# Performance work log

Hardware: AMD Instinct MI355X
Metric: run time of the kernel (lower is better)

The kernel has to match this reference:

```python
import jax, jax.numpy as jnp
import numpy as np

K = 16          # max_points
S = 3           # num_scales
DM = 256        # d_model
KD = 16         # k_dim geometric projection
TAU = 1e-4
LN_EPS = 1e-5


def _boundaries():
    edges = [(i, j) for i in range(K) for j in range(i + 1, K)]
    tris = [(i, j, k) for i in range(K) for j in range(i + 1, K) for k in range(j + 1, K)]
    E, T = len(edges), len(tris)
    B1 = np.zeros((K, E), np.float32)
    for e, (i, j) in enumerate(edges):
        B1[i, e] = -1.0
        B1[j, e] = 1.0
    eidx = {e: n for n, e in enumerate(edges)}
    B2 = np.zeros((E, T), np.float32)
    for t, (i, j, k) in enumerate(tris):
        B2[eidx[(j, k)], t] = 1.0
        B2[eidx[(i, k)], t] = -1.0
        B2[eidx[(i, j)], t] = 1.0
    ei = np.array([e[0] for e in edges])
    ej = np.array([e[1] for e in edges])
    tij = np.array([eidx[(a, b)] for a, b, c in tris])
    tjk = np.array([eidx[(b, c)] for a, b, c in tris])
    tik = np.array([eidx[(a, c)] for a, b, c in tris])
    return (jnp.asarray(B1), jnp.asarray(B2), jnp.asarray(np.abs(B1)),
            jnp.asarray(ei), jnp.asarray(ej), jnp.asarray(tij), jnp.asarray(tjk), jnp.asarray(tik))

_B1, _B2, _ABS, _EI, _EJ, _TIJ, _TJK, _TIK = _boundaries()
E = _B1.shape[1]  # 120


def _ln(x, g, b):
    m = jnp.mean(x, -1, keepdims=True)
    v = jnp.mean((x - m) ** 2, -1, keepdims=True)
    return (x - m) * jax.lax.rsqrt(v + LN_EPS) * g + b


def setup_inputs() -> dict:
    key = jax.random.key(0)
    ks = jax.random.split(key, 12)
    B = 1024
    p = lambda k, *sh: 0.02 * jax.random.normal(k, sh, dtype=jnp.float32)
    return {
        'x': jax.random.normal(ks[0], (B, K, DM), dtype=jnp.float32),
        'mask': jnp.ones((B, K), dtype=jnp.float32),
        'Wg': p(ks[1], DM, KD), 'bg': jnp.zeros((KD,), jnp.float32),
        'log_scales': jnp.linspace(-1.5, 1.5, S, dtype=jnp.float32),
        'Wv': p(ks[2], DM, DM * S), 'bv': jnp.zeros((DM * S,), jnp.float32),
        'We': p(ks[3], DM, DM * S), 'be': jnp.zeros((DM * S,), jnp.float32),
        'Wo': p(ks[4], DM * S * 2, DM), 'bo': jnp.zeros((DM,), jnp.float32),
        'ln1_g': jnp.ones((DM,), jnp.float32), 'ln1_b': jnp.zeros((DM,), jnp.float32),
        'ln2_g': jnp.ones((DM,), jnp.float32), 'ln2_b': jnp.zeros((DM,), jnp.float32),
        'Wf1': p(ks[5], DM, DM * 4), 'bf1': jnp.zeros((DM * 4,), jnp.float32),
        'Wf2': p(ks[6], DM * 4, DM), 'bf2': jnp.zeros((DM,), jnp.float32),
    }


def reference(x, mask, Wg, bg, log_scales, Wv, bv, We, be, Wo, bo,
              ln1_g, ln1_b, ln2_g, ln2_b, Wf1, bf1, Wf2, bf2):
    B = x.shape[0]
    xn = _ln(x, ln1_g, ln1_b)
    P = xn @ Wg + bg                                   # [B,K,KD]
    m2 = mask[:, :, None] * mask[:, None, :]           # [B,K,K]
    p2 = jnp.sum(P * P, -1)
    Dsq = jnp.maximum(p2[:, :, None] + p2[:, None, :] - 2.0 * jnp.einsum('bkc,blc->bkl', P, P), 0.0) * m2
    sig2 = jnp.exp(log_scales) ** 2                    # [S]
    V0 = (xn @ Wv + bv).reshape(B, K, S, DM).transpose(0, 2, 1, 3)   # [B,S,K,D]
    Eraw = jnp.einsum('ke,bkd->bed', _ABS, xn)         # [B,E,D]
    Ein = (Eraw @ We + be).reshape(B, E, S, DM).transpose(0, 2, 1, 3)  # [B,S,E,D]
    aff = jnp.exp(-Dsq[:, None] / (2.0 * sig2[None, :, None, None] + 1e-8)) * m2[:, None]  # [B,S,K,K]
    W1 = aff[:, :, _EI, _EJ]                           # [B,S,E]
    W2 = W1[:, :, _TIJ] * W1[:, :, _TJK] * W1[:, :, _TIK]  # [B,S,T]
    L0 = jnp.einsum('ke,bse,le->bskl', _B1, W1, _B1) + TAU * jnp.eye(K, dtype=x.dtype)
    node_upd = jnp.einsum('bskl,bsld->bskd', L0, V0)
    term_down = jnp.einsum('ke,bk,kf->bef', _B1, mask, _B1)
    term_up = jnp.einsum('et,bst,ft->bsef', _B2, W2, _B2)
    L1 = term_down[:, None] + term_up + TAU * jnp.eye(E, dtype=x.dtype)
    edge_msg = jnp.einsum('bsef,bsfd->bsed', L1, Ein)
    edge_upd = jnp.einsum('ke,bsed->bskd', _ABS, edge_msg)
    nu = node_upd.transpose(0, 2, 1, 3).reshape(B, K, S * DM)
    eu = edge_upd.transpose(0, 2, 1, 3).reshape(B, K, S * DM)
    x = x + (jnp.concatenate([nu, eu], -1) @ Wo + bo)  # residual + attn_out (dropout=eval noop)
    h = _ln(x, ln2_g, ln2_b)
    return x + (jax.nn.gelu(h @ Wf1 + bf1, approximate=False) @ Wf2 + bf2)
```

## Files before the change

kernel.cpp:

```cpp
#include <hip/hip_runtime.h>
#include <hip/hip_bf16.h>
#include <cstdint>
#include <cstddef>

#define TAU 1e-4f
#define LN_EPS 1e-5f

typedef unsigned short ushort_t;
typedef unsigned int uint_t;
typedef __attribute__((ext_vector_type(8))) short short8;
typedef __attribute__((ext_vector_type(4))) float f32x4;

__device__ __forceinline__ ushort_t f2bf(float f) {
    union { float f; unsigned int u; } c; c.f = f;
    unsigned int r = (c.u + 0x7fffu + ((c.u >> 16) & 1u)) >> 16;
    return (ushort_t)r;
}
__device__ __forceinline__ float bf2f(ushort_t u) {
    union { unsigned int u; float f; } c; c.u = ((unsigned int)u) << 16;
    return c.f;
}
__device__ __forceinline__ void glds16(const void* g, void* l) {
    __builtin_amdgcn_global_load_lds((const __attribute__((address_space(1))) unsigned int*)g,
                                     (__attribute__((address_space(3))) unsigned int*)l,
                                     16, 0, 0);
}

__global__ __launch_bounds__(256) void kprep(
    const float* __restrict__ Wv, const float* __restrict__ We,
    const float* __restrict__ Wo, const float* __restrict__ bv,
    const float* __restrict__ be, const float* __restrict__ Wf1,
    const float* __restrict__ Wf2, ushort_t* __restrict__ WkT,
    ushort_t* __restrict__ Wf1T, ushort_t* __restrict__ Wf2T,
    float* __restrict__ cvpart, float* __restrict__ beWo) {
    __shared__ __align__(16) float S[64 * 65];
    const int tid = threadIdx.x;
    const int id = blockIdx.x;
    if (id < 384) {
        float (*rowS)[256] = (float(*)[256])S;
        const int q0 = (id & 63) * 4;
        const int w = id >> 6;
        const int half = w / 3, s = w - half * 3;
        const float* src = half ? We : Wv;
#pragma unroll
        for (int r = 0; r < 4; ++r)
            rowS[r][tid] = src[(size_t)(q0 + r) * 768 + s * 256 + tid];
        __syncthreads();
        const float* wo = Wo + (size_t)(half * 768 + s * 256) * 256 + tid;
        float a0 = 0.f, a1 = 0.f, a2 = 0.f, a3 = 0.f;
        for (int d = 0; d < 256; ++d) {
            float wv = wo[(size_t)d * 256];
            a0 += rowS[0][d] * wv; a1 += rowS[1][d] * wv;
            a2 += rowS[2][d] * wv; a3 += rowS[3][d] * wv;
        }
        const int rt = half * 3 + s;
        ushort4 pk;
        pk.x = f2bf(a0); pk.y = f2bf(a1); pk.z = f2bf(a2); pk.w = f2bf(a3);
        *(ushort4*)&WkT[(size_t)(rt * 256 + tid) * 256 + q0] = pk;
    } else if (id < 390) {
        const int w = id - 384;
        const int half = w / 3, s = w - half * 3;
        const float* vec = half ? be : bv;
        S[tid] = vec[s * 256 + tid];
        __syncthreads();
        const float* wo = Wo + (size_t)(half * 768 + s * 256) * 256 + tid;
        float acc = 0.f;
        for (int d = 0; d < 256; ++d) acc += S[d] * wo[(size_t)d * 256];
        if (half) beWo[s * 256 + tid] = acc;
        else cvpart[s * 256 + tid] = acc;
    } else {
        float (*tS)[65] = (float(*)[65])S;
        const float* src; ushort_t* dst;
        int sr0, sc0, ss, dr0, dc0, ds_;
        if (id < 454) {
            int t = id - 390; int ki = t & 3, ni = t >> 2;
            src = Wf1; ss = 1024; sr0 = ki * 64; sc0 = ni * 64;
            dst = Wf1T; ds_ = 256; dr0 = ni * 64; dc0 = ki * 64;
        } else {
            int t = id - 454; int ki = t >> 2, ni = t & 3;
            src = Wf2; ss = 256; sr0 = ki * 64; sc0 = ni * 64;
            dst = Wf2T; ds_ = 1024; dr0 = ni * 64; dc0 = ki * 64;
        }
        const int rl = tid >> 6, cl = tid & 63;
#pragma unroll
        for (int p = 0; p < 16; ++p) {
            int r = p * 4 + rl;
            tS[r][cl] = src[(size_t)(sr0 + r) * ss + sc0 + cl];
        }
        __syncthreads();
#pragma unroll
        for (int p = 0; p < 16; ++p) {
            int r = p * 4 + rl;
            dst[(size_t)(dr0 + r) * ds_ + dc0 + cl] = f2bf(tS[cl][r]);
        }
    }
}

__global__ __launch_bounds__(256) void kLN1G(
    const float* __restrict__ xg, const float* __restrict__ maskg,
    const float* __restrict__ Wg, const float* __restrict__ bg,
    const float* __restrict__ ls, const float* __restrict__ g1,
    const float* __restrict__ b1, ushort_t* __restrict__ xnbuf,
    float* __restrict__ Mbuf, float* __restrict__ gbuf) {
    __shared__ float XS[16][260];
    __shared__ __align__(16) float WB[16 * 260];
    __shared__ float Pl[16][17];
    __shared__ float dotm[16][17];
    __shared__ float mk[16];
    float (*WgT)[260] = (float(*)[260])WB;
    float (*DsqS)[17] = (float(*)[17])WB;
    float (*Wh)[16][17] = (float(*)[16][17])(WB + 272);
    float* Ts = WB + 1088;
    const int b = blockIdx.x;
    const int tid = threadIdx.x;

    const float* xb = xg + (size_t)b * 4096;
#pragma unroll
    for (int i = 0; i < 4; ++i) {
        int idx = tid * 4 + i * 1024;
        int k = idx >> 8, c = idx & 255;
        float4 v = *(const float4*)&xb[idx];
        XS[k][c] = v.x; XS[k][c + 1] = v.y; XS[k][c + 2] = v.z; XS[k][c + 3] = v.w;
    }
    {
        const float4* wgp = (const float4*)(Wg + tid * 16);
        float4 w0 = wgp[0], w1 = wgp[1], w2 = wgp[2], w3 = wgp[3];
        WgT[0][tid] = w0.x; WgT[1][tid] = w0.y; WgT[2][tid] = w0.z; WgT[3][tid] = w0.w;
        WgT[4][tid] = w1.x; WgT[5][tid] = w1.y; WgT[6][tid] = w1.z; WgT[7][tid] = w1.w;
        WgT[8][tid] = w2.x; WgT[9][tid] = w2.y; WgT[10][tid] = w2.z; WgT[11][tid] = w2.w;
        WgT[12][tid] = w3.x; WgT[13][tid] = w3.y; WgT[14][tid] = w3.z; WgT[15][tid] = w3.w;
    }
    if (tid < 16) mk[tid] = maskg[b * 16 + tid];
    __syncthreads();

    {
        const int k = tid >> 4, c = tid & 15;
        float s = 0.f;
#pragma unroll
        for (int j = 0; j < 16; ++j) s += XS[k][c + 16 * j];
        for (int off = 8; off; off >>= 1) s += __shfl_down(s, off, 16);
        float mean = __shfl(s, 0, 16) * (1.f / 256.f);
        float vs = 0.f;
#pragma unroll
        for (int j = 0; j < 16; ++j) { float d = XS[k][c + 16 * j] - mean; vs += d * d; }
        for (int off = 8; off; off >>= 1) vs += __shfl_down(vs, off, 16);
        float rstd = rsqrtf(__shfl(vs, 0, 16) * (1.f / 256.f) + LN_EPS);
#pragma unroll
        for (int j = 0; j < 16; ++j) {
            int cc = c + 16 * j;
            XS[k][cc] = (XS[k][cc] - mean) * rstd * g1[cc] + b1[cc];
        }
    }
    __syncthreads();

#pragma unroll
    for (int i = 0; i < 8; ++i) {
        int idx2 = tid * 2 + i * 512;
        int k = idx2 >> 8, c = idx2 & 255;
        uint_t v = (uint_t)f2bf(XS[k][c]) | ((uint_t)f2bf(XS[k][c + 1]) << 16);
        *(uint_t*)&xnbuf[(size_t)b * 4096 + idx2] = v;
    }

    {
        const int k = tid >> 4, c = tid & 15;
        float acc = bg[c];
#pragma unroll
        for (int q4 = 0; q4 < 64; ++q4) {
            float4 wv = *(const float4*)&WgT[c][q4 * 4];
            float4 xv = *(const float4*)&XS[k][q4 * 4];
            acc += wv.x * xv.x + wv.y * xv.y + wv.z * xv.z + wv.w * xv.w;
        }
        Pl[k][c] = acc;
    }
    __syncthreads();
    const int k = tid >> 4, m = tid & 15;
    {
        float d = 0.f;
#pragma unroll
        for (int c = 0; c < 16; ++c) d += Pl[k][c] * Pl[m][c];
        dotm[k][m] = d;
    }
    __syncthreads();
    {
        float v = dotm[k][k] + dotm[m][m] - 2.f * dotm[k][m];
        DsqS[k][m] = fmaxf(v, 0.f) * mk[k] * mk[m];
    }
    {
        float d = DsqS[k][m];
        float mm = mk[k] * mk[m];
#pragma unroll
        for (int s = 0; s < 3; ++s) {
            float i2 = 1.f / (2.f * expf(2.f * ls[s]) + 1e-8f);
            Wh[s][k][m] = (k == m) ? 0.f : expf(-d * i2) * mm;
        }
    }
    __syncthreads();
    if (tid < 48) {
        int s = tid >> 4, j = tid & 15;
        float t = 0.f;
        for (int i = 0; i < j; ++i) {
            float d = 0.f;
            for (int jj = j + 1; jj < 16; ++jj) d += Wh[s][j][jj] * Wh[s][i][jj];
            t += Wh[s][i][j] * d;
        }
        Ts[s * 16 + j] = t;
    }
    __syncthreads();
    float gd = 0.f;
#pragma unroll
    for (int o = 0; o < 16; ++o) {
        if (o == m) continue;
        int u = o < m ? o : m, v = o < m ? m : o;
        float gu = (u == k) ? (float)(2 * k - 15) : ((u > k) ? 1.f : -1.f);
        float gv = (v == k) ? (float)(2 * k - 15) : ((v > k) ? 1.f : -1.f);
        gd += -gu * mk[u] + gv * mk[v];
        if (u == k || v == k) gd += TAU;
    }
    float* mb = Mbuf + (size_t)b * 1536;
#pragma unroll
    for (int s = 0; s < 3; ++s) {
        float rs = 0.f;
#pragma unroll
        for (int o = 0; o < 16; ++o) rs += Wh[s][k][o];
        float l0 = (k == m) ? (rs + TAU) : -Wh[s][k][m];
        float G = gd + ((k == m) ? 4.f * Ts[s * 16 + k] : 0.f);
        mb[s * 256 + tid] = l0;
        mb[768 + s * 256 + tid] = G;
        float gg = G;
        for (int off = 8; off; off >>= 1) gg += __shfl_down(gg, off, 16);
        if (m == 0) gbuf[b * 48 + k * 3 + s] = 0.5f * gg;
    }
}

__device__ __forceinline__ void gemm128(const ushort_t* __restrict__ A,
                                        const ushort_t* __restrict__ Bt,
                                        int Kdim, int m0, int n0,
                                        f32x4 acc[4][4],
                                        ushort_t (*As)[32], ushort_t (*Bs)[32]) {
    const int tid = threadIdx.x;
    const int wave = tid >> 6, lane = tid & 63;
    const int lq = lane >> 4, lr = lane & 15;
    const int wm = wave >> 1, wn = wave & 1;
    const int r = tid >> 2, ca = (tid & 3) << 3;
    const ushort_t* Ag0 = A + (size_t)(m0 + r) * Kdim + ca;
    const ushort_t* Ag1 = A + (size_t)(m0 + 64 + r) * Kdim + ca;
    const ushort_t* Bg0 = Bt + (size_t)(n0 + r) * Kdim + ca;
    const ushort_t* Bg1 = Bt + (size_t)(n0 + 64 + r) * Kdim + ca;
    char* AsD0 = (char*)As + wave * 1024;
    char* AsD1 = (char*)As + 4096 + wave * 1024;
    char* BsD0 = (char*)Bs + wave * 1024;
    char* BsD1 = (char*)Bs + 4096 + wave * 1024;
    for (int kt = 0; kt < Kdim; kt += 32) {
        __syncthreads();
        glds16(Ag0 + kt, AsD0);
        glds16(Ag1 + kt, AsD1);
        glds16(Bg0 + kt, BsD0);
        glds16(Bg1 + kt, BsD1);
        __syncthreads();
        short8 af[4], bfr[4];
#pragma unroll
        for (int i = 0; i < 4; ++i) af[i] = *(const short8*)&As[wm * 64 + i * 16 + lr][lq * 8];
#pragma unroll
        for (int j = 0; j < 4; ++j) bfr[j] = *(const short8*)&Bs[wn * 64 + j * 16 + lr][lq * 8];
#pragma unroll
        for (int i = 0; i < 4; ++i)
#pragma unroll
            for (int j = 0; j < 4; ++j)
                acc[i][j] = __builtin_amdgcn_mfma_f32_16x16x32_bf16(af[i], bfr[j], acc[i][j], 0, 0, 0);
    }
}

__device__ __forceinline__ void gemm64(const ushort_t* __restrict__ A,
                                       const ushort_t* __restrict__ Bt,
                                       int Kdim, int m0, int n0,
                                       f32x4 acc[2][4],
                                       ushort_t (*As)[32], ushort_t (*Bs)[32]) {
    const int tid = threadIdx.x;
    const int wave = tid >> 6, lane = tid & 63;
    const int lq = lane >> 4, lr = lane & 15;
    const int wm = wave >> 1, wn = wave & 1;
    const int r = tid >> 2, ca = (tid & 3) << 3;
    const ushort_t* Ag = A + (size_t)(m0 + r) * Kdim + ca;
    const ushort_t* Bg0 = Bt + (size_t)(n0 + r) * Kdim + ca;
    const ushort_t* Bg1 = Bt + (size_t)(n0 + 64 + r) * Kdim + ca;
    char* AsD = (char*)As + wave * 1024;
    char* Bs0D = (char*)Bs + wave * 1024;
    char* Bs1D = (char*)Bs + 4096 + wave * 1024;
    for (int kt = 0; kt < Kdim; kt += 32) {
        __syncthreads();
        glds16(Ag + kt, AsD);
        glds16(Bg0 + kt, Bs0D);
        glds16(Bg1 + kt, Bs1D);
        __syncthreads();
        short8 af[2], bfr[4];
#pragma unroll
        for (int i = 0; i < 2; ++i) af[i] = *(const short8*)&As[wm * 32 + i * 16 + lr][lq * 8];
#pragma unroll
        for (int j = 0; j < 4; ++j) bfr[j] = *(const short8*)&Bs[wn * 64 + j * 16 + lr][lq * 8];
#pragma unroll
        for (int i = 0; i < 2; ++i)
#pragma unroll
            for (int j = 0; j < 4; ++j)
                acc[i][j] = __builtin_amdgcn_mfma_f32_16x16x32_bf16(af[i], bfr[j], acc[i][j], 0, 0, 0);
    }
}

__global__ __launch_bounds__(256) void kY_gemm(const ushort_t* __restrict__ xn,
                                               const ushort_t* __restrict__ WkT,
                                               ushort_t* __restrict__ Y) {
    __shared__ ushort_t As[128][32];
    __shared__ ushort_t Bs[128][32];
    const int tid = threadIdx.x;
    const int m0 = blockIdx.x * 128, n0 = blockIdx.y * 128;
    f32x4 acc[4][4] = {};
    gemm128(xn, WkT, 256, m0, n0, acc, As, Bs);
    const int wave = tid >> 6, lane = tid & 63, lq = lane >> 4, lr = lane & 15;
    const int wm = wave >> 1, wn = wave & 1;
#pragma unroll
    for (int i = 0; i < 4; ++i)
#pragma unroll
        for (int j = 0; j < 4; ++j) {
            int n = n0 + wn * 64 + j * 16 + lr;
#pragma unroll
            for (int v = 0; v < 4; ++v) {
                int rg = m0 + wm * 64 + i * 16 + lq * 4 + v;
                Y[(size_t)rg * 1536 + n] = f2bf(acc[i][j][v]);
            }
        }
}

__global__ __launch_bounds__(256) void kZ_apply(
    const ushort_t* __restrict__ Y, const float* __restrict__ Mbuf,
    const float* __restrict__ xin, const float* __restrict__ bo,
    const float* __restrict__ cvpart, const float* __restrict__ beWo,
    const float* __restrict__ gbuf, const float* __restrict__ g2,
    const float* __restrict__ b2, float* __restrict__ xp,
    ushort_t* __restrict__ h) {
    __shared__ __align__(16) char YsRaw[49152];
    ushort_t* Ys = (ushort_t*)YsRaw;
    float (*xpS)[260] = (float(*)[260])YsRaw;
    __shared__ float Ms[1536];
    __shared__ float gS[48];
    __shared__ float mrS[16][2];
    const int b = blockIdx.x, tid = threadIdx.x;
    const int wave = tid >> 6, lane = tid & 63;
    const char* Ybc = (const char*)(Y + (size_t)b * 24576);
#pragma unroll
    for (int it = 0; it < 12; ++it) {
        int base = it * 4096 + wave * 1024;
        glds16(Ybc + base + lane * 16, YsRaw + base);
    }
#pragma unroll
    for (int i = 0; i < 6; ++i) Ms[tid + i * 256] = Mbuf[(size_t)b * 1536 + tid + i * 256];
    if (tid < 48) gS[tid] = gbuf[b * 48 + tid];
    __syncthreads();

    const int q = tid;
    float yv[96];
#pragma unroll
    for (int rt = 0; rt < 6; ++rt)
#pragma unroll
        for (int l = 0; l < 16; ++l)
            yv[rt * 16 + l] = bf2f(Ys[l * 1536 + rt * 256 + q]);

    float accv[16];
#pragma unroll
    for (int k = 0; k < 16; ++k) {
        float a = 0.f;
#pragma unroll
        for (int rt = 0; rt < 6; ++rt) {
            const float4* mp = (const float4*)&Ms[rt * 256 + k * 16];
            float4 m0 = mp[0], m1 = mp[1], m2 = mp[2], m3 = mp[3];
            const float* yp = &yv[rt * 16];
            a += m0.x * yp[0] + m0.y * yp[1] + m0.z * yp[2] + m0.w * yp[3]
               + m1.x * yp[4] + m1.y * yp[5] + m1.z * yp[6] + m1.w * yp[7]
               + m2.x * yp[8] + m2.y * yp[9] + m2.z * yp[10] + m2.w * yp[11]
               + m3.x * yp[12] + m3.y * yp[13] + m3.z * yp[14] + m3.w * yp[15];
        }
        accv[k] = a;
    }

    float cv = bo[q] + TAU * (cvpart[q] + cvpart[256 + q] + cvpart[512 + q]);
    float bw0 = beWo[q], bw1 = beWo[256 + q], bw2 = beWo[512 + q];
    const float* xb2 = xin + (size_t)b * 4096;
    float* xpb = xp + (size_t)b * 4096;
    float xpv[16];
#pragma unroll
    for (int k = 0; k < 16; ++k) {
        xpv[k] = accv[k] + xb2[k * 256 + q] + cv +
                 gS[k * 3] * bw0 + gS[k * 3 + 1] * bw1 + gS[k * 3 + 2] * bw2;
        xpb[k * 256 + q] = xpv[k];
    }
    __syncthreads();
#pragma unroll
    for (int k = 0; k < 16; ++k) xpS[k][q] = xpv[k];
    __syncthreads();

    {
        const int kk = tid >> 4, c = tid & 15;
        float s = 0.f;
#pragma unroll
        for (int j = 0; j < 16; ++j) s += xpS[kk][c + 16 * j];
        for (int off = 8; off; off >>= 1) s += __shfl_down(s, off, 16);
        float mean = __shfl(s, 0, 16) * (1.f / 256.f);
        float vs = 0.f;
#pragma unroll
        for (int j = 0; j < 16; ++j) { float d = xpS[kk][c + 16 * j] - mean; vs += d * d; }
        for (int off = 8; off; off >>= 1) vs += __shfl_down(vs, off, 16);
        float rstd = rsqrtf(__shfl(vs, 0, 16) * (1.f / 256.f) + LN_EPS);
        if (c == 0) { mrS[kk][0] = mean; mrS[kk][1] = rstd; }
    }
    __syncthreads();
    ushort_t* hb = h + (size_t)b * 4096;
    const float g2q = g2[q], b2q = b2[q];
#pragma unroll
    for (int k = 0; k < 16; ++k) {
        float m = mrS[k][0], r = mrS[k][1];
        hb[k * 256 + q] = f2bf((xpS[k][q] - m) * r * g2q + b2q);
    }
}

__global__ __launch_bounds__(256) void k3_gemm(const ushort_t* __restrict__ h,
                                               const ushort_t* __restrict__ Wf1T,
                                               const float* __restrict__ bf1,
                                               ushort_t* __restrict__ F1g) {
    __shared__ ushort_t As[128][32];
    __shared__ ushort_t Bs[128][32];
    const int tid = threadIdx.x;
    const int m0 = blockIdx.x * 128, n0 = blockIdx.y * 128;
    f32x4 acc[4][4] = {};
    gemm128(h, Wf1T, 256, m0, n0, acc, As, Bs);
    const int wave = tid >> 6, lane = tid & 63, lq = lane >> 4, lr = lane & 15;
    const int wm = wave >> 1, wn = wave & 1;
#pragma unroll
    for (int i = 0; i < 4; ++i)
#pragma unroll
        for (int j = 0; j < 4; ++j) {
            int n = n0 + wn * 64 + j * 16 + lr;
            float bn = bf1[n];
#pragma unroll
            for (int v = 0; v < 4; ++v) {
                int rg = m0 + wm * 64 + i * 16 + lq * 4 + v;
                float u = acc[i][j][v] + bn;
                float gl = 0.5f * u * (1.f + erff(u * 0.70710678118f));
                F1g[(size_t)rg * 1024 + n] = f2bf(gl);
            }
        }
}

__global__ __launch_bounds__(256) void k4_gemm(const ushort_t* __restrict__ F1g,
                                               const ushort_t* __restrict__ Wf2T,
                                               const float* __restrict__ bf2,
                                               const float* __restrict__ xp,
                                               float* __restrict__ out) {
    __shared__ ushort_t As[64][32];
    __shared__ ushort_t Bs[128][32];
    const int tid = threadIdx.x;
    const int m0 = blockIdx.x * 64, n0 = blockIdx.y * 128;
    f32x4 acc[2][4] = {};
    gemm64(F1g, Wf2T, 1024, m0, n0, acc, As, Bs);
    const int wave = tid >> 6, lane = tid & 63, lq = lane >> 4, lr = lane & 15;
    const int wm = wave >> 1, wn = wave & 1;
#pragma unroll
    for (int i = 0; i < 2; ++i)
#pragma unroll
        for (int j = 0; j < 4; ++j) {
            int n = n0 + wn * 64 + j * 16 + lr;
            float bn = bf2[n];
#pragma unroll
            for (int v = 0; v < 4; ++v) {
                size_t idx = (size_t)(m0 + wm * 32 + i * 16 + lq * 4 + v) * 256 + n;
                out[idx] = xp[idx] + acc[i][j][v] + bn;
            }
        }
}

extern "C" void kernel_launch(void* const* d_in, const int* in_sizes, int n_in,
                              void* d_out, int out_size, void* d_ws, size_t ws_size,
                              hipStream_t stream) {
    const float* x = (const float*)d_in[0];
    const float* mask = (const float*)d_in[1];
    const float* Wg = (const float*)d_in[2];
    const float* bg = (const float*)d_in[3];
    const float* ls = (const float*)d_in[4];
    const float* Wv = (const float*)d_in[5];
    const float* bv = (const float*)d_in[6];
    const float* We = (const float*)d_in[7];
    const float* be = (const float*)d_in[8];
    const float* Wo = (const float*)d_in[9];
    const float* bo = (const float*)d_in[10];
    const float* g1 = (const float*)d_in[11];
    const float* b1 = (const float*)d_in[12];
    const float* g2 = (const float*)d_in[13];
    const float* b2 = (const float*)d_in[14];
    const float* Wf1 = (const float*)d_in[15];
    const float* bf1 = (const float*)d_in[16];
    const float* Wf2 = (const float*)d_in[17];
    const float* bf2 = (const float*)d_in[18];
    float* out = (float*)d_out;

    char* ws = (char*)d_ws;
    ushort_t* Y = (ushort_t*)(ws);
    ushort_t* F1g = (ushort_t*)(ws);
    ushort_t* WkT = (ushort_t*)(ws + 50331648);
    ushort_t* Wf1T = (ushort_t*)(ws + 51118080);
    ushort_t* Wf2T = (ushort_t*)(ws + 51642368);
    float* cvpart = (float*)(ws + 52166656);
    float* beWo = (float*)(ws + 52169728);
    float* gbuf = (float*)(ws + 52172800);
    float* xp = (float*)(ws + 52369408);
    ushort_t* h = (ushort_t*)(ws + 69146624);
    ushort_t* xnbuf = (ushort_t*)(ws + 77535232);
    float* Mbuf = (float*)(ws + 85923840);

    kprep<<<dim3(518), dim3(256), 0, stream>>>(Wv, We, Wo, bv, be, Wf1, Wf2,
                                               WkT, Wf1T, Wf2T, cvpart, beWo);
    kLN1G<<<dim3(1024), dim3(256), 0, stream>>>(x, mask, Wg, bg, ls, g1, b1,
                                                xnbuf, Mbuf, gbuf);
    kY_gemm<<<dim3(128, 12), dim3(256), 0, stream>>>(xnbuf, WkT, Y);
    kZ_apply<<<dim3(1024), dim3(256), 0, stream>>>(Y, Mbuf, x, bo, cvpart, beWo, gbuf, g2, b2, xp, h);
    k3_gemm<<<dim3(128, 8), dim3(256), 0, stream>>>(h, Wf1T, bf1, F1g);
    k4_gemm<<<dim3(256, 2), dim3(256), 0, stream>>>(F1g, Wf2T, bf2, xp, out);
}
```

Measured before the change: 235.6 us.

## Fuse LN2 and both FFN GEMMs into one kernel; merge prep with LN1

Merges the weight-prep kernel and the LN1/geometry kernel into one launch, dispatched by block index. Moves LayerNorm2 out of kZ_apply into a new kFFN kernel. kFFN keeps the normalized rows in LDS, computes the 1024-wide GELU hidden layer in 128-column chunks, and feeds each chunk straight into the second GEMM, so the bf16 hidden activations never go to global memory. This removes two launches and the h/F1g round-trips. In exchange, the FFN grid shrinks to 256 blocks, each running long serial chunk loops with many barriers, which lowers parallelism on a large-CU GPU.

```diff
diff --git a/kernel.cpp b/kernel.cpp
--- a/kernel.cpp
+++ b/kernel.cpp
@@ -26,93 +26,94 @@
                                      16, 0, 0);
 }
 
-__global__ __launch_bounds__(256) void kprep(
+__global__ __launch_bounds__(256) void kA(
+    const float* __restrict__ xg, const float* __restrict__ maskg,
+    const float* __restrict__ Wg, const float* __restrict__ bg,
+    const float* __restrict__ ls, const float* __restrict__ g1,
+    const float* __restrict__ b1, ushort_t* __restrict__ xnbuf,
+    float* __restrict__ Mbuf, float* __restrict__ gbuf,
     const float* __restrict__ Wv, const float* __restrict__ We,
     const float* __restrict__ Wo, const float* __restrict__ bv,
     const float* __restrict__ be, const float* __restrict__ Wf1,
     const float* __restrict__ Wf2, ushort_t* __restrict__ WkT,
     ushort_t* __restrict__ Wf1T, ushort_t* __restrict__ Wf2T,
     float* __restrict__ cvpart, float* __restrict__ beWo) {
-    __shared__ __align__(16) float S[64 * 65];
+    __shared__ __align__(16) float POOL[8880];
     const int tid = threadIdx.x;
-    const int id = blockIdx.x;
-    if (id < 384) {
-        float (*rowS)[256] = (float(*)[256])S;
-        const int q0 = (id & 63) * 4;
-        const int w = id >> 6;
-        const int half = w / 3, s = w - half * 3;
-        const float* src = half ? We : Wv;
-#pragma unroll
-        for (int r = 0; r < 4; ++r)
-            rowS[r][tid] = src[(size_t)(q0 + r) * 768 + s * 256 + tid];
-        __syncthreads();
-        const float* wo = Wo + (size_t)(half * 768 + s * 256) * 256 + tid;
-        float a0 = 0.f, a1 = 0.f, a2 = 0.f, a3 = 0.f;
-        for (int d = 0; d < 256; ++d) {
-            float wv = wo[(size_t)d * 256];
-            a0 += rowS[0][d] * wv; a1 += rowS[1][d] * wv;
-            a2 += rowS[2][d] * wv; a3 += rowS[3][d] * wv;
-        }
-        const int rt = half * 3 + s;
-        ushort4 pk;
-        pk.x = f2bf(a0); pk.y = f2bf(a1); pk.z = f2bf(a2); pk.w = f2bf(a3);
-        *(ushort4*)&WkT[(size_t)(rt * 256 + tid) * 256 + q0] = pk;
-    } else if (id < 390) {
-        const int w = id - 384;
-        const int half = w / 3, s = w - half * 3;
-        const float* vec = half ? be : bv;
-        S[tid] = vec[s * 256 + tid];
-        __syncthreads();
-        const float* wo = Wo + (size_t)(half * 768 + s * 256) * 256 + tid;
-        float acc = 0.f;
-        for (int d = 0; d < 256; ++d) acc += S[d] * wo[(size_t)d * 256];
-        if (half) beWo[s * 256 + tid] = acc;
-        else cvpart[s * 256 + tid] = acc;
-    } else {
-        float (*tS)[65] = (float(*)[65])S;
-        const float* src; ushort_t* dst;
-        int sr0, sc0, ss, dr0, dc0, ds_;
-        if (id < 454) {
-            int t = id - 390; int ki = t & 3, ni = t >> 2;
-            src = Wf1; ss = 1024; sr0 = ki * 64; sc0 = ni * 64;
-            dst = Wf1T; ds_ = 256; dr0 = ni * 64; dc0 = ki * 64;
+
+    if (blockIdx.x >= 1024) {
+        const int id = blockIdx.x - 1024;
+        if (id < 384) {
+            float (*rowS)[256] = (float(*)[256])POOL;
+            const int q0 = (id & 63) * 4;
+            const int w = id >> 6;
+            const int half = w / 3, s = w - half * 3;
+            const float* src = half ? We : Wv;
+#pragma unroll
+            for (int r = 0; r < 4; ++r)
+                rowS[r][tid] = src[(size_t)(q0 + r) * 768 + s * 256 + tid];
+            __syncthreads();
+            const float* wo = Wo + (size_t)(half * 768 + s * 256) * 256 + tid;
+            float a0 = 0.f, a1 = 0.f, a2 = 0.f, a3 = 0.f;
+            for (int d = 0; d < 256; ++d) {
+                float wv = wo[(size_t)d * 256];
+                a0 += rowS[0][d] * wv; a1 += rowS[1][d] * wv;
+                a2 += rowS[2][d] * wv; a3 += rowS[3][d] * wv;
+            }
+            const int rt = half * 3 + s;
+            ushort4 pk;
+            pk.x = f2bf(a0); pk.y = f2bf(a1); pk.z = f2bf(a2); pk.w = f2bf(a3);
+            *(ushort4*)&WkT[(size_t)(rt * 256 + tid) * 256 + q0] = pk;
+        } else if (id < 390) {
+            const int w = id - 384;
+            const int half = w / 3, s = w - half * 3;
+            const float* vec = half ? be : bv;
+            POOL[tid] = vec[s * 256 + tid];
+            __syncthreads();
+            const float* wo = Wo + (size_t)(half * 768 + s * 256) * 256 + tid;
+            float acc = 0.f;
+            for (int d = 0; d < 256; ++d) acc += POOL[d] * wo[(size_t)d * 256];
+            if (half) beWo[s * 256 + tid] = acc;
+            else cvpart[s * 256 + tid] = acc;
         } else {
-            int t = id - 454; int ki = t >> 2, ni = t & 3;
-            src = Wf2; ss = 256; sr0 = ki * 64; sc0 = ni * 64;
-            dst = Wf2T; ds_ = 1024; dr0 = ni * 64; dc0 = ki * 64;
-        }
-        const int rl = tid >> 6, cl = tid & 63;
-#pragma unroll
-        for (int p = 0; p < 16; ++p) {
-            int r = p * 4 + rl;
-            tS[r][cl] = src[(size_t)(sr0 + r) * ss + sc0 + cl];
-        }
-        __syncthreads();
-#pragma unroll
-        for (int p = 0; p < 16; ++p) {
-            int r = p * 4 + rl;
-            dst[(size_t)(dr0 + r) * ds_ + dc0 + cl] = f2bf(tS[cl][r]);
-        }
-    }
-}
-
-__global__ __launch_bounds__(256) void kLN1G(
-    const float* __restrict__ xg, const float* __restrict__ maskg,
-    const float* __restrict__ Wg, const float* __restrict__ bg,
-    const float* __restrict__ ls, const float* __restrict__ g1,
-    const float* __restrict__ b1, ushort_t* __restrict__ xnbuf,
-    float* __restrict__ Mbuf, float* __restrict__ gbuf) {
-    __shared__ float XS[16][260];
-    __shared__ __align__(16) float WB[16 * 260];
-    __shared__ float Pl[16][17];
-    __shared__ float dotm[16][17];
-    __shared__ float mk[16];
+            float (*tS)[65] = (float(*)[65])POOL;
+            const float* src; ushort_t* dst;
+            int sr0, sc0, ss, dr0, dc0, ds_;
+            if (id < 454) {
+                int t = id - 390; int ki = t & 3, ni = t >> 2;
+                src = Wf1; ss = 1024; sr0 = ki * 64; sc0 = ni * 64;
+                dst = Wf1T; ds_ = 256; dr0 = ni * 64; dc0 = ki * 64;
+            } else {
+                int t = id - 454; int ki = t >> 2, ni = t & 3;
+                src = Wf2; ss = 256; sr0 = ki * 64; sc0 = ni * 64;
+                dst = Wf2T; ds_ = 1024; dr0 = ni * 64; dc0 = ki * 64;
+            }
+            const int rl = tid >> 6, cl = tid & 63;
+#pragma unroll
+            for (int p = 0; p < 16; ++p) {
+                int r = p * 4 + rl;
+                tS[r][cl] = src[(size_t)(sr0 + r) * ss + sc0 + cl];
+            }
+            __syncthreads();
+#pragma unroll
+            for (int p = 0; p < 16; ++p) {
+                int r = p * 4 + rl;
+                dst[(size_t)(dr0 + r) * ds_ + dc0 + cl] = f2bf(tS[cl][r]);
+            }
+        }
+        return;
+    }
+
+    const int b = blockIdx.x;
+    float (*XS)[260] = (float(*)[260])POOL;
+    float* WB = POOL + 4160;
+    float (*Pl)[17] = (float(*)[17])(POOL + 8320);
+    float (*dotm)[17] = (float(*)[17])(POOL + 8592);
+    float* mk = POOL + 8864;
     float (*WgT)[260] = (float(*)[260])WB;
     float (*DsqS)[17] = (float(*)[17])WB;
     float (*Wh)[16][17] = (float(*)[16][17])(WB + 272);
     float* Ts = WB + 1088;
-    const int b = blockIdx.x;
-    const int tid = threadIdx.x;
 
     const float* xb = xg + (size_t)b * 4096;
 #pragma unroll
@@ -270,41 +271,6 @@
     }
 }
 
-__device__ __forceinline__ void gemm64(const ushort_t* __restrict__ A,
-                                       const ushort_t* __restrict__ Bt,
-                                       int Kdim, int m0, int n0,
-                                       f32x4 acc[2][4],
-                                       ushort_t (*As)[32], ushort_t (*Bs)[32]) {
-    const int tid = threadIdx.x;
-    const int wave = tid >> 6, lane = tid & 63;
-    const int lq = lane >> 4, lr = lane & 15;
-    const int wm = wave >> 1, wn = wave & 1;
-    const int r = tid >> 2, ca = (tid & 3) << 3;
-    const ushort_t* Ag = A + (size_t)(m0 + r) * Kdim + ca;
-    const ushort_t* Bg0 = Bt + (size_t)(n0 + r) * Kdim + ca;
-    const ushort_t* Bg1 = Bt + (size_t)(n0 + 64 + r) * Kdim + ca;
-    char* AsD = (char*)As + wave * 1024;
-    char* Bs0D = (char*)Bs + wave * 1024;
-    char* Bs1D = (char*)Bs + 4096 + wave * 1024;
-    for (int kt = 0; kt < Kdim; kt += 32) {
-        __syncthreads();
-        glds16(Ag + kt, AsD);
-        glds16(Bg0 + kt, Bs0D);
-        glds16(Bg1 + kt, Bs1D);
-        __syncthreads();
-        short8 af[2], bfr[4];
-#pragma unroll
-        for (int i = 0; i < 2; ++i) af[i] = *(const short8*)&As[wm * 32 + i * 16 + lr][lq * 8];
-#pragma unroll
-        for (int j = 0; j < 4; ++j) bfr[j] = *(const short8*)&Bs[wn * 64 + j * 16 + lr][lq * 8];
-#pragma unroll
-        for (int i = 0; i < 2; ++i)
-#pragma unroll
-            for (int j = 0; j < 4; ++j)
-                acc[i][j] = __builtin_amdgcn_mfma_f32_16x16x32_bf16(af[i], bfr[j], acc[i][j], 0, 0, 0);
-    }
-}
-
 __global__ __launch_bounds__(256) void kY_gemm(const ushort_t* __restrict__ xn,
                                                const ushort_t* __restrict__ WkT,
                                                ushort_t* __restrict__ Y) {
@@ -333,15 +299,11 @@
     const ushort_t* __restrict__ Y, const float* __restrict__ Mbuf,
     const float* __restrict__ xin, const float* __restrict__ bo,
     const float* __restrict__ cvpart, const float* __restrict__ beWo,
-    const float* __restrict__ gbuf, const float* __restrict__ g2,
-    const float* __restrict__ b2, float* __restrict__ xp,
-    ushort_t* __restrict__ h) {
+    const float* __restrict__ gbuf, float* __restrict__ xp) {
     __shared__ __align__(16) char YsRaw[49152];
     ushort_t* Ys = (ushort_t*)YsRaw;
-    float (*xpS)[260] = (float(*)[260])YsRaw;
     __shared__ float Ms[1536];
     __shared__ float gS[48];
-    __shared__ float mrS[16][2];
     const int b = blockIdx.x, tid = threadIdx.x;
     const int wave = tid >> 6, lane = tid & 63;
     const char* Ybc = (const char*)(Y + (size_t)b * 24576);
@@ -384,93 +346,136 @@
     float bw0 = beWo[q], bw1 = beWo[256 + q], bw2 = beWo[512 + q];
     const float* xb2 = xin + (size_t)b * 4096;
     float* xpb = xp + (size_t)b * 4096;
-    float xpv[16];
 #pragma unroll
     for (int k = 0; k < 16; ++k) {
-        xpv[k] = accv[k] + xb2[k * 256 + q] + cv +
-                 gS[k * 3] * bw0 + gS[k * 3 + 1] * bw1 + gS[k * 3 + 2] * bw2;
-        xpb[k * 256 + q] = xpv[k];
-    }
-    __syncthreads();
-#pragma unroll
-    for (int k = 0; k < 16; ++k) xpS[k][q] = xpv[k];
-    __syncthreads();
-
-    {
-        const int kk = tid >> 4, c = tid & 15;
+        xpb[k * 256 + q] = accv[k] + xb2[k * 256 + q] + cv +
+                           gS[k * 3] * bw0 + gS[k * 3 + 1] * bw1 + gS[k * 3 + 2] * bw2;
+    }
+}
+
+__global__ __launch_bounds__(256) void kFFN(
+    const float* __restrict__ xp, const ushort_t* __restrict__ Wf1T,
+    const float* __restrict__ bf1, const ushort_t* __restrict__ Wf2T,
+    const float* __restrict__ bf2, const float* __restrict__ g2,
+    const float* __restrict__ b2, float* __restrict__ out) {
+    __shared__ ushort_t hS[8][64][34];
+    __shared__ ushort_t F1S[4][64][34];
+    __shared__ ushort_t Bs1[128][32];
+    __shared__ ushort_t Bs2[256][32];
+    __shared__ float g2S[256], b2S[256], bf2S[256], bf1S[1024];
+    const int tid = threadIdx.x;
+    const int wave = tid >> 6, lane = tid & 63;
+    const int lq = lane >> 4, lr = lane & 15;
+    const int m0 = blockIdx.x * 64;
+
+    g2S[tid] = g2[tid]; b2S[tid] = b2[tid]; bf2S[tid] = bf2[tid];
+#pragma unroll
+    for (int i = 0; i < 4; ++i) bf1S[tid + i * 256] = bf1[tid + i * 256];
+
+    {
+        const int r = tid >> 2, c4 = tid & 3;
+        const float* xr = xp + (size_t)(m0 + r) * 256 + c4 * 64;
+        float vals[64];
         float s = 0.f;
 #pragma unroll
-        for (int j = 0; j < 16; ++j) s += xpS[kk][c + 16 * j];
-        for (int off = 8; off; off >>= 1) s += __shfl_down(s, off, 16);
-        float mean = __shfl(s, 0, 16) * (1.f / 256.f);
-        float vs = 0.f;
-#pragma unroll
-        for (int j = 0; j < 16; ++j) { float d = xpS[kk][c + 16 * j] - mean; vs += d * d; }
-        for (int off = 8; off; off >>= 1) vs += __shfl_down(vs, off, 16);
-        float rstd = rsqrtf(__shfl(vs, 0, 16) * (1.f / 256.f) + LN_EPS);
-        if (c == 0) { mrS[kk][0] = mean; mrS[kk][1] = rstd; }
-    }
-    __syncthreads();
-    ushort_t* hb = h + (size_t)b * 4096;
-    const float g2q = g2[q], b2q = b2[q];
-#pragma unroll
-    for (int k = 0; k < 16; ++k) {
-        float m = mrS[k][0], r = mrS[k][1];
-        hb[k * 256 + q] = f2bf((xpS[k][q] - m) * r * g2q + b2q);
-    }
-}
-
-__global__ __launch_bounds__(256) void k3_gemm(const ushort_t* __restrict__ h,
-                                               const ushort_t* __restrict__ Wf1T,
-                                               const float* __restrict__ bf1,
-                                               ushort_t* __restrict__ F1g) {
-    __shared__ ushort_t As[128][32];
-    __shared__ ushort_t Bs[128][32];
-    const int tid = threadIdx.x;
-    const int m0 = blockIdx.x * 128, n0 = blockIdx.y * 128;
-    f32x4 acc[4][4] = {};
-    gemm128(h, Wf1T, 256, m0, n0, acc, As, Bs);
-    const int wave = tid >> 6, lane = tid & 63, lq = lane >> 4, lr = lane & 15;
-    const int wm = wave >> 1, wn = wave & 1;
+        for (int i = 0; i < 16; ++i) {
+            float4 v = *(const float4*)(xr + i * 4);
+            vals[i * 4 + 0] = v.x; vals[i * 4 + 1] = v.y;
+            vals[i * 4 + 2] = v.z; vals[i * 4 + 3] = v.w;
+            s += (v.x + v.y) + (v.z + v.w);
+        }
+        s += __shfl_xor(s, 1, 64); s += __shfl_xor(s, 2, 64);
+        float mean = s * (1.f / 256.f);
+        float q = 0.f;
+#pragma unroll
+        for (int i = 0; i < 64; ++i) { float d = vals[i] - mean; q += d * d; }
+        q += __shfl_xor(q, 1, 64); q += __shfl_xor(q, 2, 64);
+        float rstd = rsqrtf(q * (1.f / 256.f) + LN_EPS);
+        __syncthreads();
+#pragma unroll
+        for (int i = 0; i < 32; ++i) {
+            int col = c4 * 64 + i * 2;
+            float h0 = (vals[i * 2] - mean) * rstd * g2S[col] + b2S[col];
+            float h1 = (vals[i * 2 + 1] - mean) * rstd * g2S[col + 1] + b2S[col + 1];
+            uint_t pk = (uint_t)f2bf(h0) | ((uint_t)f2bf(h1) << 16);
+            *(uint_t*)&hS[col >> 5][r][col & 31] = pk;
+        }
+    }
+    __syncthreads();
+
+    const int wm2 = wave >> 1, wn2 = wave & 1;
+    const int rS = tid >> 2, caS = (tid & 3) << 3;
+    f32x4 acc2[4][4] = {};
+    for (int nc = 0; nc < 8; ++nc) {
+        f32x4 acc1[2][4] = {};
+        const ushort_t* Bg0 = Wf1T + (size_t)(nc * 128 + rS) * 256 + caS;
+        const ushort_t* Bg1 = Wf1T + (size_t)(nc * 128 + 64 + rS) * 256 + caS;
+        for (int kt = 0; kt < 256; kt += 32) {
+            __syncthreads();
+            glds16(Bg0 + kt, (char*)Bs1 + wave * 1024);
+            glds16(Bg1 + kt, (char*)Bs1 + 4096 + wave * 1024);
+            __syncthreads();
+            const int kti = kt >> 5;
+            short8 af[2], bfv[4];
+#pragma unroll
+            for (int i = 0; i < 2; ++i)
+                af[i] = *(const short8*)&hS[kti][wm2 * 32 + i * 16 + lr][lq * 8];
+#pragma unroll
+            for (int j = 0; j < 4; ++j)
+                bfv[j] = *(const short8*)&Bs1[wn2 * 64 + j * 16 + lr][lq * 8];
+#pragma unroll
+            for (int i = 0; i < 2; ++i)
+#pragma unroll
+                for (int j = 0; j < 4; ++j)
+                    acc1[i][j] = __builtin_amdgcn_mfma_f32_16x16x32_bf16(af[i], bfv[j], acc1[i][j], 0, 0, 0);
+        }
+        __syncthreads();
+#pragma unroll
+        for (int i = 0; i < 2; ++i)
+#pragma unroll
+            for (int j = 0; j < 4; ++j) {
+                int colc = wn2 * 64 + j * 16 + lr;
+                float bn = bf1S[nc * 128 + colc];
+#pragma unroll
+                for (int v = 0; v < 4; ++v) {
+                    int row = wm2 * 32 + i * 16 + lq * 4 + v;
+                    float u = acc1[i][j][v] + bn;
+                    float gl = 0.5f * u * (1.f + erff(u * 0.70710678118f));
+                    F1S[colc >> 5][row][colc & 31] = f2bf(gl);
+                }
+            }
+        __syncthreads();
+        for (int kt2 = 0; kt2 < 4; ++kt2) {
+            __syncthreads();
+            const ushort_t* Bg = Wf2T + (size_t)rS * 1024 + nc * 128 + kt2 * 32 + caS;
+#pragma unroll
+            for (int c = 0; c < 4; ++c)
+                glds16(Bg + (size_t)c * 64 * 1024, (char*)Bs2 + c * 4096 + wave * 1024);
+            __syncthreads();
+            short8 af2[4], bfv2[4];
+#pragma unroll
+            for (int i = 0; i < 4; ++i)
+                af2[i] = *(const short8*)&F1S[kt2][i * 16 + lr][lq * 8];
+#pragma unroll
+            for (int j = 0; j < 4; ++j)
+                bfv2[j] = *(const short8*)&Bs2[wave * 64 + j * 16 + lr][lq * 8];
+#pragma unroll
+            for (int i = 0; i < 4; ++i)
+#pragma unroll
+                for (int j = 0; j < 4; ++j)
+                    acc2[i][j] = __builtin_amdgcn_mfma_f32_16x16x32_bf16(af2[i], bfv2[j], acc2[i][j], 0, 0, 0);
+        }
+    }
 #pragma unroll
     for (int i = 0; i < 4; ++i)
 #pragma unroll
         for (int j = 0; j < 4; ++j) {
-            int n = n0 + wn * 64 + j * 16 + lr;
-            float bn = bf1[n];
+            int n = wave * 64 + j * 16 + lr;
+            float bn = bf2S[n];
 #pragma unroll
             for (int v = 0; v < 4; ++v) {
-                int rg = m0 + wm * 64 + i * 16 + lq * 4 + v;
-                float u = acc[i][j][v] + bn;
-                float gl = 0.5f * u * (1.f + erff(u * 0.70710678118f));
-                F1g[(size_t)rg * 1024 + n] = f2bf(gl);
-            }
-        }
-}
-
-__global__ __launch_bounds__(256) void k4_gemm(const ushort_t* __restrict__ F1g,
-                                               const ushort_t* __restrict__ Wf2T,
-                                               const float* __restrict__ bf2,
-                                               const float* __restrict__ xp,
-                                               float* __restrict__ out) {
-    __shared__ ushort_t As[64][32];
-    __shared__ ushort_t Bs[128][32];
-    const int tid = threadIdx.x;
-    const int m0 = blockIdx.x * 64, n0 = blockIdx.y * 128;
-    f32x4 acc[2][4] = {};
-    gemm64(F1g, Wf2T, 1024, m0, n0, acc, As, Bs);
-    const int wave = tid >> 6, lane = tid & 63, lq = lane >> 4, lr = lane & 15;
-    const int wm = wave >> 1, wn = wave & 1;
-#pragma unroll
-    for (int i = 0; i < 2; ++i)
-#pragma unroll
-        for (int j = 0; j < 4; ++j) {
-            int n = n0 + wn * 64 + j * 16 + lr;
-            float bn = bf2[n];
-#pragma unroll
-            for (int v = 0; v < 4; ++v) {
-                size_t idx = (size_t)(m0 + wm * 32 + i * 16 + lq * 4 + v) * 256 + n;
-                out[idx] = xp[idx] + acc[i][j][v] + bn;
+                size_t idx = (size_t)(m0 + i * 16 + lq * 4 + v) * 256 + n;
+                out[idx] = xp[idx] + acc2[i][j][v] + bn;
             }
         }
 }
@@ -501,7 +506,6 @@
 
     char* ws = (char*)d_ws;
     ushort_t* Y = (ushort_t*)(ws);
-    ushort_t* F1g = (ushort_t*)(ws);
     ushort_t* WkT = (ushort_t*)(ws + 50331648);
     ushort_t* Wf1T = (ushort_t*)(ws + 51118080);
     ushort_t* Wf2T = (ushort_t*)(ws + 51642368);
@@ -509,16 +513,14 @@
     float* beWo = (float*)(ws + 52169728);
     float* gbuf = (float*)(ws + 52172800);
     float* xp = (float*)(ws + 52369408);
-    ushort_t* h = (ushort_t*)(ws + 69146624);
     ushort_t* xnbuf = (ushort_t*)(ws + 77535232);
     float* Mbuf = (float*)(ws + 85923840);
 
-    kprep<<<dim3(518), dim3(256), 0, stream>>>(Wv, We, Wo, bv, be, Wf1, Wf2,
-                                               WkT, Wf1T, Wf2T, cvpart, beWo);
-    kLN1G<<<dim3(1024), dim3(256), 0, stream>>>(x, mask, Wg, bg, ls, g1, b1,
-                                                xnbuf, Mbuf, gbuf);
+    kA<<<dim3(1542), dim3(256), 0, stream>>>(x, mask, Wg, bg, ls, g1, b1,
+                                             xnbuf, Mbuf, gbuf,
+                                             Wv, We, Wo, bv, be, Wf1, Wf2,
+                                             WkT, Wf1T, Wf2T, cvpart, beWo);
     kY_gemm<<<dim3(128, 12), dim3(256), 0, stream>>>(xnbuf, WkT, Y);
-    kZ_apply<<<dim3(1024), dim3(256), 0, stream>>>(Y, Mbuf, x, bo, cvpart, beWo, gbuf, g2, b2, xp, h);
-    k3_gemm<<<dim3(128, 8), dim3(256), 0, stream>>>(h, Wf1T, bf1, F1g);
-    k4_gemm<<<dim3(256, 2), dim3(256), 0, stream>>>(F1g, Wf2T, bf2, xp, out);
-}
+    kZ_apply<<<dim3(1024), dim3(256), 0, stream>>>(Y, Mbuf, x, bo, cvpart, beWo, gbuf, xp);
+    kFFN<<<dim3(256), dim3(256), 0, stream>>>(xp, Wf1T, bf1, Wf2T, bf2, g2, b2, out);
+}
```

Result: slower. 248.6 us (+5.5%).
